# Kernel optimization log

Measured on AMD Instinct MI355X. Metric: run time of the kernel, lower is better.

## Reference

```python
import jax, jax.numpy as jnp
import numpy as np

N, T, HID, H = 2, 2048, 1024, 16
D = HID // H


def setup_inputs() -> dict:
    key = jax.random.key(0)
    ks = jax.random.split(key, 11)
    s = 1.0 / np.sqrt(HID)
    return {
        "q": jax.random.normal(ks[0], (N, T, HID), jnp.float32),
        "k": jax.random.normal(ks[1], (N, T, HID), jnp.float32),
        "v": jax.random.normal(ks[2], (N, T, HID), jnp.float32),
        "Wq": jax.random.normal(ks[3], (HID, HID), jnp.float32) * s,
        "bq": jnp.zeros((HID,), jnp.float32),
        "Wk": jax.random.normal(ks[4], (HID, HID), jnp.float32) * s,
        "bk": jnp.zeros((HID,), jnp.float32),
        "Wv": jax.random.normal(ks[5], (HID, HID), jnp.float32) * s,
        "bv": jnp.zeros((HID,), jnp.float32),
        "Wo": jax.random.normal(ks[6], (HID, HID), jnp.float32) * s,
        "bo": jnp.zeros((HID,), jnp.float32),
    }


def reference(q, k, v, Wq, bq, Wk, bk, Wv, bv, Wo, bo):
    n, t, _ = q.shape
    # Linear projections, then the original's quirky head split:
    # .view(N, H, T, D) directly from (N, T, H*D) (no transpose).
    qh = (q @ Wq + bq).reshape(n, H, t, D)
    kh = (k @ Wk + bk).reshape(n, H, t, D)
    vh = (v @ Wv + bv).reshape(n, H, t, D)
    # scores: (N, H, T, T), scaled by sqrt(hidden_size) (not head dim)
    scores = jnp.einsum("nhtd,nhsd->nhts", qh, kh) / jnp.sqrt(jnp.float32(HID))
    # faithful quirk: softmax over dim=1 (the head axis)
    attn = jax.nn.softmax(scores, axis=1)
    # dropout is identity (eval / drop_rate=0)
    out = jnp.einsum("nhts,nhsd->nhtd", attn, vh).reshape(n, t, H * D)
    return out @ Wo + bo
```

## Files before the change

kernel.cpp:

```cpp
#include <hip/hip_runtime.h>

typedef unsigned short u16;
typedef __bf16 bf16x8 __attribute__((ext_vector_type(8)));
typedef float f32x4 __attribute__((ext_vector_type(4)));

#define MFMA16 __builtin_amdgcn_mfma_f32_16x16x32_bf16

constexpr int NB = 2, TS = 2048, HD = 1024, NH = 16, DH = 64;
constexpr float SCALE = 0.03125f;

__device__ __forceinline__ u16 f2bf(float f) {
    union { float f; unsigned u; } v; v.f = f;
    unsigned r = v.u + 0x7FFFu + ((v.u >> 16) & 1u);
    return (u16)(r >> 16);
}
__device__ __forceinline__ float bf2f(u16 h) {
    union { unsigned u; float f; } v; v.u = ((unsigned)h) << 16;
    return v.f;
}
__device__ __forceinline__ bf16x8 ldb8(const u16* p) {
    return *reinterpret_cast<const bf16x8*>(p);
}
__device__ __forceinline__ void glds16(const u16* g, u16* l) {
    __builtin_amdgcn_global_load_lds(
        (const __attribute__((address_space(1))) unsigned int*)g,
        (__attribute__((address_space(3))) unsigned int*)l, 16, 0, 0);
}

__global__ __launch_bounds__(256) void to_bf16(
    const float* __restrict__ a0, const float* __restrict__ a1, const float* __restrict__ a2,
    u16* __restrict__ o0, u16* __restrict__ o1, u16* __restrict__ o2)
{
    const float* s; u16* d;
    if (blockIdx.y == 0)      { s = a0; d = o0; }
    else if (blockIdx.y == 1) { s = a1; d = o1; }
    else                      { s = a2; d = o2; }
    size_t i = ((size_t)blockIdx.x * 256 + threadIdx.x) * 8;
    float4 v0 = *reinterpret_cast<const float4*>(s + i);
    float4 v1 = *reinterpret_cast<const float4*>(s + i + 4);
    u16 t[8] = { f2bf(v0.x), f2bf(v0.y), f2bf(v0.z), f2bf(v0.w),
                 f2bf(v1.x), f2bf(v1.y), f2bf(v1.z), f2bf(v1.w) };
    *reinterpret_cast<uint4*>(d + i) = *reinterpret_cast<const uint4*>(t);
}

__global__ __launch_bounds__(256) void wtrans(
    const float* __restrict__ w0, const float* __restrict__ w1,
    const float* __restrict__ w2, const float* __restrict__ w3,
    u16* __restrict__ o0, u16* __restrict__ o1,
    u16* __restrict__ o2, u16* __restrict__ o3)
{
    const float* src; u16* dst;
    if (blockIdx.z == 0)      { src = w0; dst = o0; }
    else if (blockIdx.z == 1) { src = w1; dst = o1; }
    else if (blockIdx.z == 2) { src = w2; dst = o2; }
    else                      { src = w3; dst = o3; }
    __shared__ __align__(16) u16 tile[64 * 72];
    const int k0 = blockIdx.y * 64, n0 = blockIdx.x * 64;
    const int t = threadIdx.x, r = t >> 2, c0 = (t & 3) << 4;
#pragma unroll
    for (int j = 0; j < 4; ++j) {
        float4 v = *reinterpret_cast<const float4*>(&src[(size_t)(k0 + r) * HD + n0 + c0 + 4 * j]);
        tile[(c0 + 4 * j + 0) * 72 + r] = f2bf(v.x);
        tile[(c0 + 4 * j + 1) * 72 + r] = f2bf(v.y);
        tile[(c0 + 4 * j + 2) * 72 + r] = f2bf(v.z);
        tile[(c0 + 4 * j + 3) * 72 + r] = f2bf(v.w);
    }
    __syncthreads();
#pragma unroll
    for (int j = 0; j < 2; ++j)
        *reinterpret_cast<uint4*>(&dst[(size_t)(n0 + r) * HD + k0 + c0 + 8 * j]) =
            *reinterpret_cast<const uint4*>(&tile[r * 72 + c0 + 8 * j]);
}

template <typename OT>
__global__ __launch_bounds__(256) void gemm_bt(
    const u16* __restrict__ A, const u16* __restrict__ BT,
    const float* __restrict__ bias, OT* __restrict__ C,
    int M, int N, int K)
{
    __shared__ __align__(16) u16 As[64 * 32];
    __shared__ __align__(16) u16 Bs[128 * 32];
    const int m0 = blockIdx.y * 64, n0 = blockIdx.x * 128;
    const int tid = threadIdx.x, wid = tid >> 6, lane = tid & 63;
    const int q = lane >> 4, c = lane & 15;
    const int wm = wid >> 1, wn = wid & 1;
    const int arow = tid >> 2, acol = (tid & 3) << 3;
    f32x4 acc[2][4] = {};
    for (int k0 = 0; k0 < K; k0 += 32) {
        glds16(&A[(size_t)(m0 + arow) * K + k0 + acol], &As[tid * 8]);
        glds16(&BT[(size_t)(n0 + arow) * K + k0 + acol], &Bs[tid * 8]);
        glds16(&BT[(size_t)(n0 + 64 + arow) * K + k0 + acol], &Bs[2048 + tid * 8]);
        __syncthreads();
        bf16x8 af[2], bf[4];
#pragma unroll
        for (int jm = 0; jm < 2; ++jm) af[jm] = ldb8(&As[(wm * 32 + jm * 16 + c) * 32 + q * 8]);
#pragma unroll
        for (int jn = 0; jn < 4; ++jn) bf[jn] = ldb8(&Bs[(wn * 64 + jn * 16 + c) * 32 + q * 8]);
#pragma unroll
        for (int jm = 0; jm < 2; ++jm)
#pragma unroll
            for (int jn = 0; jn < 4; ++jn)
                acc[jm][jn] = MFMA16(af[jm], bf[jn], acc[jm][jn], 0, 0, 0);
        __syncthreads();
    }
#pragma unroll
    for (int jm = 0; jm < 2; ++jm)
#pragma unroll
        for (int jn = 0; jn < 4; ++jn) {
            int row = m0 + wm * 32 + jm * 16 + q * 4;
            int col = n0 + wn * 64 + jn * 16 + c;
            float b = bias[col];
#pragma unroll
            for (int r = 0; r < 4; ++r) {
                float v = acc[jm][jn][r] + b;
                if constexpr (sizeof(OT) == 4)
                    reinterpret_cast<float*>(C)[(size_t)(row + r) * N + col] = v;
                else
                    reinterpret_cast<u16*>(C)[(size_t)(row + r) * N + col] = f2bf(v);
            }
        }
}

__global__ __launch_bounds__(256) void vtrans(const u16* __restrict__ V, u16* __restrict__ VT)
{
    __shared__ __align__(16) u16 tile[64 * 72];
    const int nh = blockIdx.y, t0 = blockIdx.x * 64;
    const u16* src = V + (size_t)nh * TS * DH;
    u16* dst = VT + (size_t)nh * DH * TS;
    const int t = threadIdx.x, r = t >> 2, c0 = (t & 3) << 4;
    *reinterpret_cast<uint4*>(&tile[r * 72 + c0]) =
        *reinterpret_cast<const uint4*>(&src[(size_t)(t0 + r) * DH + c0]);
    *reinterpret_cast<uint4*>(&tile[r * 72 + c0 + 8]) =
        *reinterpret_cast<const uint4*>(&src[(size_t)(t0 + r) * DH + c0 + 8]);
    __syncthreads();
    const int d = t >> 2, tc = (t & 3) << 4;
    u16 tmp[16];
#pragma unroll
    for (int j = 0; j < 16; ++j) tmp[j] = tile[(tc + j) * 72 + d];
    *reinterpret_cast<uint4*>(&dst[(size_t)d * TS + t0 + tc]) = *reinterpret_cast<const uint4*>(&tmp[0]);
    *reinterpret_cast<uint4*>(&dst[(size_t)d * TS + t0 + tc + 8]) = *reinterpret_cast<const uint4*>(&tmp[8]);
}

__global__ __launch_bounds__(256) void z_kernel(
    const u16* __restrict__ Qp, const u16* __restrict__ Kp, u16* __restrict__ Zf)
{
    __shared__ __align__(16) u16 Ks[64 * 64];
    const int sb = blockIdx.x, tb = blockIdx.y, n = blockIdx.z;
    const int s0 = sb * 64, t0 = tb * 128;
    const int tid = threadIdx.x, wid = tid >> 6, lane = tid & 63;
    const int q = lane >> 4, c = lane & 15;
    const int krow = tid >> 3, kch = tid & 7;
    float zacc[2][4][4] = {};
    for (int h = 0; h < NH; ++h) {
        const u16* Qh = Qp + (size_t)(n * NH + h) * TS * DH;
        const u16* Kh = Kp + (size_t)(n * NH + h) * TS * DH;
        glds16(&Kh[(size_t)(s0 + krow) * DH + ((kch ^ (krow & 7)) << 3)], &Ks[tid * 8]);
        glds16(&Kh[(size_t)(s0 + 32 + krow) * DH + ((kch ^ (krow & 7)) << 3)], &Ks[2048 + tid * 8]);
        __syncthreads();
        bf16x8 qa[2][2], kb[4][2];
#pragma unroll
        for (int jm = 0; jm < 2; ++jm)
#pragma unroll
            for (int kf = 0; kf < 2; ++kf)
                qa[jm][kf] = ldb8(&Qh[(size_t)(t0 + wid * 32 + jm * 16 + c) * DH + kf * 32 + q * 8]);
#pragma unroll
        for (int i = 0; i < 4; ++i)
#pragma unroll
            for (int kf = 0; kf < 2; ++kf)
                kb[i][kf] = ldb8(&Ks[(i * 16 + c) * 64 + (((kf * 4 + q) ^ (c & 7)) << 3)]);
        f32x4 s_[2][4] = {};
#pragma unroll
        for (int kf = 0; kf < 2; ++kf)
#pragma unroll
            for (int jm = 0; jm < 2; ++jm)
#pragma unroll
                for (int i = 0; i < 4; ++i)
                    s_[jm][i] = MFMA16(qa[jm][kf], kb[i][kf], s_[jm][i], 0, 0, 0);
#pragma unroll
        for (int jm = 0; jm < 2; ++jm)
#pragma unroll
            for (int i = 0; i < 4; ++i)
#pragma unroll
                for (int r = 0; r < 4; ++r)
                    zacc[jm][i][r] += __expf(s_[jm][i][r] * SCALE);
        __syncthreads();
    }
    size_t chunk = ((size_t)((n * 32 + sb) * 16 + tb)) * 8192 + wid * 2048 + lane * 32;
#pragma unroll
    for (int jm = 0; jm < 2; ++jm) {
        u16 w_[16];
#pragma unroll
        for (int i = 0; i < 4; ++i)
#pragma unroll
            for (int r = 0; r < 4; ++r)
                w_[i * 4 + r] = f2bf(1.0f / zacc[jm][i][r]);
        *reinterpret_cast<uint4*>(&Zf[chunk + jm * 16])     = *reinterpret_cast<const uint4*>(&w_[0]);
        *reinterpret_cast<uint4*>(&Zf[chunk + jm * 16 + 8]) = *reinterpret_cast<const uint4*>(&w_[8]);
    }
}

__global__ __launch_bounds__(256) void attn_kernel(
    const u16* __restrict__ Qp, const u16* __restrict__ Kp, const u16* __restrict__ VT,
    const u16* __restrict__ Zf, u16* __restrict__ o2)
{
    __shared__ __align__(16) u16 Ks[64 * 64];
    __shared__ __align__(16) u16 Vs[64 * 64];
    __shared__ __align__(16) u16 Ps[128 * 72];
    const int tb = blockIdx.x, h = blockIdx.y, n = blockIdx.z;
    const int t0 = tb * 128;
    const int tid = threadIdx.x, wid = tid >> 6, lane = tid & 63;
    const int q = lane >> 4, c = lane & 15;
    const int krow = tid >> 3, kch = tid & 7;
    const size_t base = (size_t)(n * NH + h) * TS * DH;
    const u16* Qh = Qp + base; const u16* Kh = Kp + base; const u16* VTh = VT + base;
    bf16x8 qa[2][2];
#pragma unroll
    for (int jm = 0; jm < 2; ++jm)
#pragma unroll
        for (int kf = 0; kf < 2; ++kf)
            qa[jm][kf] = ldb8(&Qh[(size_t)(t0 + wid * 32 + jm * 16 + c) * DH + kf * 32 + q * 8]);
    f32x4 oacc[2][4] = {};
    for (int sb = 0; sb < 32; ++sb) {
        const int s0 = sb * 64;
        glds16(&Kh[(size_t)(s0 + krow) * DH + ((kch ^ (krow & 7)) << 3)], &Ks[tid * 8]);
        glds16(&Kh[(size_t)(s0 + 32 + krow) * DH + ((kch ^ (krow & 7)) << 3)], &Ks[2048 + tid * 8]);
        glds16(&VTh[(size_t)krow * TS + s0 + ((kch ^ (krow & 7)) << 3)], &Vs[tid * 8]);
        glds16(&VTh[(size_t)(32 + krow) * TS + s0 + ((kch ^ (krow & 7)) << 3)], &Vs[2048 + tid * 8]);
        __syncthreads();
        bf16x8 kb[4][2];
#pragma unroll
        for (int i = 0; i < 4; ++i)
#pragma unroll
            for (int kf = 0; kf < 2; ++kf)
                kb[i][kf] = ldb8(&Ks[(i * 16 + c) * 64 + (((kf * 4 + q) ^ (c & 7)) << 3)]);
        f32x4 s_[2][4] = {};
#pragma unroll
        for (int kf = 0; kf < 2; ++kf)
#pragma unroll
            for (int jm = 0; jm < 2; ++jm)
#pragma unroll
                for (int i = 0; i < 4; ++i)
                    s_[jm][i] = MFMA16(qa[jm][kf], kb[i][kf], s_[jm][i], 0, 0, 0);
        size_t chunk = ((size_t)((n * 32 + sb) * 16 + tb)) * 8192 + wid * 2048 + lane * 32;
        u16 zl[32];
        *reinterpret_cast<uint4*>(&zl[0])  = *reinterpret_cast<const uint4*>(&Zf[chunk]);
        *reinterpret_cast<uint4*>(&zl[8])  = *reinterpret_cast<const uint4*>(&Zf[chunk + 8]);
        *reinterpret_cast<uint4*>(&zl[16]) = *reinterpret_cast<const uint4*>(&Zf[chunk + 16]);
        *reinterpret_cast<uint4*>(&zl[24]) = *reinterpret_cast<const uint4*>(&Zf[chunk + 24]);
#pragma unroll
        for (int jm = 0; jm < 2; ++jm)
#pragma unroll
            for (int i = 0; i < 4; ++i)
#pragma unroll
                for (int r = 0; r < 4; ++r) {
                    float p = __expf(s_[jm][i][r] * SCALE) * bf2f(zl[jm * 16 + i * 4 + r]);
                    Ps[(wid * 32 + jm * 16 + q * 4 + r) * 72 + i * 16 + c] = f2bf(p);
                }
        bf16x8 pa[2][2], vb[4][2];
#pragma unroll
        for (int jm = 0; jm < 2; ++jm)
#pragma unroll
            for (int kf = 0; kf < 2; ++kf)
                pa[jm][kf] = ldb8(&Ps[(wid * 32 + jm * 16 + c) * 72 + kf * 32 + q * 8]);
#pragma unroll
        for (int dn = 0; dn < 4; ++dn)
#pragma unroll
            for (int kf = 0; kf < 2; ++kf)
                vb[dn][kf] = ldb8(&Vs[(dn * 16 + c) * 64 + (((kf * 4 + q) ^ (c & 7)) << 3)]);
#pragma unroll
        for (int kf = 0; kf < 2; ++kf)
#pragma unroll
            for (int jm = 0; jm < 2; ++jm)
#pragma unroll
                for (int dn = 0; dn < 4; ++dn)
                    oacc[jm][dn] = MFMA16(pa[jm][kf], vb[dn][kf], oacc[jm][dn], 0, 0, 0);
        __syncthreads();
    }
#pragma unroll
    for (int jm = 0; jm < 2; ++jm)
#pragma unroll
        for (int dn = 0; dn < 4; ++dn)
#pragma unroll
            for (int r = 0; r < 4; ++r)
                o2[base + (size_t)(t0 + wid * 32 + jm * 16 + q * 4 + r) * DH + dn * 16 + c] =
                    f2bf(oacc[jm][dn][r]);
}

extern "C" void kernel_launch(void* const* d_in, const int* in_sizes, int n_in,
                              void* d_out, int out_size, void* d_ws, size_t ws_size,
                              hipStream_t stream)
{
    const float* q  = (const float*)d_in[0];
    const float* k  = (const float*)d_in[1];
    const float* v  = (const float*)d_in[2];
    const float* Wq = (const float*)d_in[3];
    const float* bq = (const float*)d_in[4];
    const float* Wk = (const float*)d_in[5];
    const float* bk = (const float*)d_in[6];
    const float* Wv = (const float*)d_in[7];
    const float* bv = (const float*)d_in[8];
    const float* Wo = (const float*)d_in[9];
    const float* bo = (const float*)d_in[10];
    float* out = (float*)d_out;

    u16* ws  = (u16*)d_ws;
    u16* wqT = ws + 0 * 1048576;
    u16* wkT = ws + 1 * 1048576;
    u16* wvT = ws + 2 * 1048576;
    u16* woT = ws + 3 * 1048576;
    u16* S1  = ws + 4194304;
    u16* S2  = S1 + 4194304;
    u16* S3  = S2 + 4194304;
    u16* S4  = S3 + 4194304;
    u16* S5  = S4 + 4194304;
    u16* qb = S1, * kb = S2, * vb = S3;
    u16* Qp = S4, * Kp = S1, * Vp = S2;
    u16* VTb = S3, * Zf = S5, * o2 = S2;

    to_bf16<<<dim3(2048, 3), 256, 0, stream>>>(q, k, v, qb, kb, vb);
    wtrans<<<dim3(16, 16, 4), 256, 0, stream>>>(Wq, Wk, Wv, Wo, wqT, wkT, wvT, woT);
    gemm_bt<u16><<<dim3(8, 64), 256, 0, stream>>>(qb, wqT, bq, Qp, NB * TS, HD, HD);
    gemm_bt<u16><<<dim3(8, 64), 256, 0, stream>>>(kb, wkT, bk, Kp, NB * TS, HD, HD);
    gemm_bt<u16><<<dim3(8, 64), 256, 0, stream>>>(vb, wvT, bv, Vp, NB * TS, HD, HD);
    vtrans<<<dim3(32, 32), 256, 0, stream>>>(Vp, VTb);
    z_kernel<<<dim3(32, 16, 2), 256, 0, stream>>>(Qp, Kp, Zf);
    attn_kernel<<<dim3(16, 16, 2), 256, 0, stream>>>(Qp, Kp, VTb, Zf, o2);
    gemm_bt<float><<<dim3(8, 64), 256, 0, stream>>>(o2, woT, bo, out, NB * TS, HD, HD);
}
```

Measured before the change: 332.7 us.

## Batch QKV projections into one larger-tile GEMM and vectorize bf16 epilogues

Merges the three Q/K/V projection GEMMs into a single launch indexed by blockIdx.z, using 128x128 tiles with 4x4 MFMA accumulators per wave for more operand reuse. Swaps MFMA operand order so each lane holds four contiguous output columns, letting epilogues write packed bf16 pairs and float4 stores instead of scattered scalar stores. Adds a packed hardware bf16 conversion helper with a software fallback, used across the conversion, Z, P and output writes. Workspace buffers are reassigned to fit the concurrent outputs, at the cost of higher register use in the larger GEMM tile.

```diff
diff --git a/kernel.cpp b/kernel.cpp
--- a/kernel.cpp
+++ b/kernel.cpp
@@ -25,6 +25,24 @@
     __builtin_amdgcn_global_load_lds(
         (const __attribute__((address_space(1))) unsigned int*)g,
         (__attribute__((address_space(3))) unsigned int*)l, 16, 0, 0);
+}
+
+#if defined(__has_builtin)
+#  if __has_builtin(__builtin_amdgcn_cvt_pk_bf16_f32)
+#    define HAVE_PKBF16 1
+#  endif
+#endif
+#ifndef HAVE_PKBF16
+#  define HAVE_PKBF16 0
+#endif
+__device__ __forceinline__ unsigned pk2(float a, float b) {
+#if HAVE_PKBF16
+    typedef __bf16 bf16x2 __attribute__((ext_vector_type(2)));
+    bf16x2 r = __builtin_amdgcn_cvt_pk_bf16_f32(a, b);
+    return __builtin_bit_cast(unsigned, r);
+#else
+    return (unsigned)f2bf(a) | ((unsigned)f2bf(b) << 16);
+#endif
 }
 
 __global__ __launch_bounds__(256) void to_bf16(
@@ -38,9 +56,8 @@
     size_t i = ((size_t)blockIdx.x * 256 + threadIdx.x) * 8;
     float4 v0 = *reinterpret_cast<const float4*>(s + i);
     float4 v1 = *reinterpret_cast<const float4*>(s + i + 4);
-    u16 t[8] = { f2bf(v0.x), f2bf(v0.y), f2bf(v0.z), f2bf(v0.w),
-                 f2bf(v1.x), f2bf(v1.y), f2bf(v1.z), f2bf(v1.w) };
-    *reinterpret_cast<uint4*>(d + i) = *reinterpret_cast<const uint4*>(t);
+    uint4 w = { pk2(v0.x, v0.y), pk2(v0.z, v0.w), pk2(v1.x, v1.y), pk2(v1.z, v1.w) };
+    *reinterpret_cast<uint4*>(d + i) = w;
 }
 
 __global__ __launch_bounds__(256) void wtrans(
@@ -72,10 +89,60 @@
             *reinterpret_cast<const uint4*>(&tile[r * 72 + c0 + 8 * j]);
 }
 
-template <typename OT>
-__global__ __launch_bounds__(256) void gemm_bt(
+__global__ __launch_bounds__(256) void gemm_qkv(
+    const u16* __restrict__ A0, const u16* __restrict__ A1, const u16* __restrict__ A2,
+    const u16* __restrict__ B0, const u16* __restrict__ B1, const u16* __restrict__ B2,
+    const float* __restrict__ c0, const float* __restrict__ c1, const float* __restrict__ c2,
+    u16* __restrict__ C0, u16* __restrict__ C1, u16* __restrict__ C2)
+{
+    const u16 *A, *BT; const float* bias; u16* C;
+    if (blockIdx.z == 0)      { A = A0; BT = B0; bias = c0; C = C0; }
+    else if (blockIdx.z == 1) { A = A1; BT = B1; bias = c1; C = C1; }
+    else                      { A = A2; BT = B2; bias = c2; C = C2; }
+    constexpr int M = NB * TS, N = HD, K = HD;
+    __shared__ __align__(16) u16 As[128 * 32];
+    __shared__ __align__(16) u16 Bs[128 * 32];
+    const int m0 = blockIdx.y * 128, n0 = blockIdx.x * 128;
+    const int tid = threadIdx.x, wid = tid >> 6, lane = tid & 63;
+    const int q = lane >> 4, c = lane & 15;
+    const int wm = wid >> 1, wn = wid & 1;
+    const int srow = tid >> 2, scol = (tid & 3) << 3;
+    (void)M;
+    f32x4 acc[4][4] = {};
+    for (int k0 = 0; k0 < K; k0 += 32) {
+        glds16(&A[(size_t)(m0 + srow) * K + k0 + scol],       &As[tid * 8]);
+        glds16(&A[(size_t)(m0 + 64 + srow) * K + k0 + scol],  &As[2048 + tid * 8]);
+        glds16(&BT[(size_t)(n0 + srow) * K + k0 + scol],      &Bs[tid * 8]);
+        glds16(&BT[(size_t)(n0 + 64 + srow) * K + k0 + scol], &Bs[2048 + tid * 8]);
+        __syncthreads();
+        bf16x8 af[4], bf[4];
+#pragma unroll
+        for (int i = 0; i < 4; ++i)  af[i] = ldb8(&As[(wm * 64 + i * 16 + c) * 32 + q * 8]);
+#pragma unroll
+        for (int jn = 0; jn < 4; ++jn) bf[jn] = ldb8(&Bs[(wn * 64 + jn * 16 + c) * 32 + q * 8]);
+#pragma unroll
+        for (int i = 0; i < 4; ++i)
+#pragma unroll
+            for (int jn = 0; jn < 4; ++jn)
+                acc[i][jn] = MFMA16(bf[jn], af[i], acc[i][jn], 0, 0, 0);
+        __syncthreads();
+    }
+#pragma unroll
+    for (int i = 0; i < 4; ++i)
+#pragma unroll
+        for (int jn = 0; jn < 4; ++jn) {
+            int row = m0 + wm * 64 + i * 16 + c;
+            int col = n0 + wn * 64 + jn * 16 + q * 4;
+            float4 bb = *reinterpret_cast<const float4*>(&bias[col]);
+            uint2 w = { pk2(acc[i][jn][0] + bb.x, acc[i][jn][1] + bb.y),
+                        pk2(acc[i][jn][2] + bb.z, acc[i][jn][3] + bb.w) };
+            *reinterpret_cast<uint2*>(&C[(size_t)row * N + col]) = w;
+        }
+}
+
+__global__ __launch_bounds__(256) void gemm_out(
     const u16* __restrict__ A, const u16* __restrict__ BT,
-    const float* __restrict__ bias, OT* __restrict__ C,
+    const float* __restrict__ bias, float* __restrict__ C,
     int M, int N, int K)
 {
     __shared__ __align__(16) u16 As[64 * 32];
@@ -100,24 +167,19 @@
         for (int jm = 0; jm < 2; ++jm)
 #pragma unroll
             for (int jn = 0; jn < 4; ++jn)
-                acc[jm][jn] = MFMA16(af[jm], bf[jn], acc[jm][jn], 0, 0, 0);
+                acc[jm][jn] = MFMA16(bf[jn], af[jm], acc[jm][jn], 0, 0, 0);
         __syncthreads();
     }
 #pragma unroll
     for (int jm = 0; jm < 2; ++jm)
 #pragma unroll
         for (int jn = 0; jn < 4; ++jn) {
-            int row = m0 + wm * 32 + jm * 16 + q * 4;
-            int col = n0 + wn * 64 + jn * 16 + c;
-            float b = bias[col];
-#pragma unroll
-            for (int r = 0; r < 4; ++r) {
-                float v = acc[jm][jn][r] + b;
-                if constexpr (sizeof(OT) == 4)
-                    reinterpret_cast<float*>(C)[(size_t)(row + r) * N + col] = v;
-                else
-                    reinterpret_cast<u16*>(C)[(size_t)(row + r) * N + col] = f2bf(v);
-            }
+            int row = m0 + wm * 32 + jm * 16 + c;
+            int col = n0 + wn * 64 + jn * 16 + q * 4;
+            float4 bb = *reinterpret_cast<const float4*>(&bias[col]);
+            float4 v = { acc[jm][jn][0] + bb.x, acc[jm][jn][1] + bb.y,
+                         acc[jm][jn][2] + bb.z, acc[jm][jn][3] + bb.w };
+            *reinterpret_cast<float4*>(&C[(size_t)row * N + col]) = v;
         }
 }
 
@@ -175,7 +237,7 @@
             for (int jm = 0; jm < 2; ++jm)
 #pragma unroll
                 for (int i = 0; i < 4; ++i)
-                    s_[jm][i] = MFMA16(qa[jm][kf], kb[i][kf], s_[jm][i], 0, 0, 0);
+                    s_[jm][i] = MFMA16(kb[i][kf], qa[jm][kf], s_[jm][i], 0, 0, 0);
 #pragma unroll
         for (int jm = 0; jm < 2; ++jm)
 #pragma unroll
@@ -188,14 +250,14 @@
     size_t chunk = ((size_t)((n * 32 + sb) * 16 + tb)) * 8192 + wid * 2048 + lane * 32;
 #pragma unroll
     for (int jm = 0; jm < 2; ++jm) {
-        u16 w_[16];
-#pragma unroll
-        for (int i = 0; i < 4; ++i)
-#pragma unroll
-            for (int r = 0; r < 4; ++r)
-                w_[i * 4 + r] = f2bf(1.0f / zacc[jm][i][r]);
-        *reinterpret_cast<uint4*>(&Zf[chunk + jm * 16])     = *reinterpret_cast<const uint4*>(&w_[0]);
-        *reinterpret_cast<uint4*>(&Zf[chunk + jm * 16 + 8]) = *reinterpret_cast<const uint4*>(&w_[8]);
+        unsigned w32[8];
+#pragma unroll
+        for (int i = 0; i < 4; ++i) {
+            w32[i * 2 + 0] = pk2(1.0f / zacc[jm][i][0], 1.0f / zacc[jm][i][1]);
+            w32[i * 2 + 1] = pk2(1.0f / zacc[jm][i][2], 1.0f / zacc[jm][i][3]);
+        }
+        *reinterpret_cast<uint4*>(&Zf[chunk + jm * 16])     = *reinterpret_cast<const uint4*>(&w32[0]);
+        *reinterpret_cast<uint4*>(&Zf[chunk + jm * 16 + 8]) = *reinterpret_cast<const uint4*>(&w32[4]);
     }
 }
 
@@ -240,7 +302,7 @@
             for (int jm = 0; jm < 2; ++jm)
 #pragma unroll
                 for (int i = 0; i < 4; ++i)
-                    s_[jm][i] = MFMA16(qa[jm][kf], kb[i][kf], s_[jm][i], 0, 0, 0);
+                    s_[jm][i] = MFMA16(kb[i][kf], qa[jm][kf], s_[jm][i], 0, 0, 0);
         size_t chunk = ((size_t)((n * 32 + sb) * 16 + tb)) * 8192 + wid * 2048 + lane * 32;
         u16 zl[32];
         *reinterpret_cast<uint4*>(&zl[0])  = *reinterpret_cast<const uint4*>(&Zf[chunk]);
@@ -250,12 +312,14 @@
 #pragma unroll
         for (int jm = 0; jm < 2; ++jm)
 #pragma unroll
-            for (int i = 0; i < 4; ++i)
-#pragma unroll
-                for (int r = 0; r < 4; ++r) {
-                    float p = __expf(s_[jm][i][r] * SCALE) * bf2f(zl[jm * 16 + i * 4 + r]);
-                    Ps[(wid * 32 + jm * 16 + q * 4 + r) * 72 + i * 16 + c] = f2bf(p);
-                }
+            for (int i = 0; i < 4; ++i) {
+                float p0 = __expf(s_[jm][i][0] * SCALE) * bf2f(zl[jm * 16 + i * 4 + 0]);
+                float p1 = __expf(s_[jm][i][1] * SCALE) * bf2f(zl[jm * 16 + i * 4 + 1]);
+                float p2 = __expf(s_[jm][i][2] * SCALE) * bf2f(zl[jm * 16 + i * 4 + 2]);
+                float p3 = __expf(s_[jm][i][3] * SCALE) * bf2f(zl[jm * 16 + i * 4 + 3]);
+                uint2 w = { pk2(p0, p1), pk2(p2, p3) };
+                *reinterpret_cast<uint2*>(&Ps[(wid * 32 + jm * 16 + c) * 72 + i * 16 + q * 4]) = w;
+            }
         bf16x8 pa[2][2], vb[4][2];
 #pragma unroll
         for (int jm = 0; jm < 2; ++jm)
@@ -273,17 +337,19 @@
             for (int jm = 0; jm < 2; ++jm)
 #pragma unroll
                 for (int dn = 0; dn < 4; ++dn)
-                    oacc[jm][dn] = MFMA16(pa[jm][kf], vb[dn][kf], oacc[jm][dn], 0, 0, 0);
+                    oacc[jm][dn] = MFMA16(vb[dn][kf], pa[jm][kf], oacc[jm][dn], 0, 0, 0);
         __syncthreads();
     }
 #pragma unroll
     for (int jm = 0; jm < 2; ++jm)
 #pragma unroll
-        for (int dn = 0; dn < 4; ++dn)
-#pragma unroll
-            for (int r = 0; r < 4; ++r)
-                o2[base + (size_t)(t0 + wid * 32 + jm * 16 + q * 4 + r) * DH + dn * 16 + c] =
-                    f2bf(oacc[jm][dn][r]);
+        for (int dn = 0; dn < 4; ++dn) {
+            int t = t0 + wid * 32 + jm * 16 + c;
+            int d = dn * 16 + q * 4;
+            uint2 w = { pk2(oacc[jm][dn][0], oacc[jm][dn][1]),
+                        pk2(oacc[jm][dn][2], oacc[jm][dn][3]) };
+            *reinterpret_cast<uint2*>(&o2[base + (size_t)t * DH + d]) = w;
+        }
 }
 
 extern "C" void kernel_launch(void* const* d_in, const int* in_sizes, int n_in,
@@ -313,17 +379,18 @@
     u16* S3  = S2 + 4194304;
     u16* S4  = S3 + 4194304;
     u16* S5  = S4 + 4194304;
-    u16* qb = S1, * kb = S2, * vb = S3;
-    u16* Qp = S4, * Kp = S1, * Vp = S2;
-    u16* VTb = S3, * Zf = S5, * o2 = S2;
+    u16* S6  = S5 + 4194304;
+    (void)S3;
+    u16 *qb = S1, *kb = S2, *vb = S3;
+    u16 *Qp = S4, *Kp = S5, *Vp = S6;
+    u16 *VTb = S1, *Zf = S2, *o2 = S6;
 
     to_bf16<<<dim3(2048, 3), 256, 0, stream>>>(q, k, v, qb, kb, vb);
     wtrans<<<dim3(16, 16, 4), 256, 0, stream>>>(Wq, Wk, Wv, Wo, wqT, wkT, wvT, woT);
-    gemm_bt<u16><<<dim3(8, 64), 256, 0, stream>>>(qb, wqT, bq, Qp, NB * TS, HD, HD);
-    gemm_bt<u16><<<dim3(8, 64), 256, 0, stream>>>(kb, wkT, bk, Kp, NB * TS, HD, HD);
-    gemm_bt<u16><<<dim3(8, 64), 256, 0, stream>>>(vb, wvT, bv, Vp, NB * TS, HD, HD);
+    gemm_qkv<<<dim3(8, 32, 3), 256, 0, stream>>>(qb, kb, vb, wqT, wkT, wvT,
+                                                 bq, bk, bv, Qp, Kp, Vp);
     vtrans<<<dim3(32, 32), 256, 0, stream>>>(Vp, VTb);
     z_kernel<<<dim3(32, 16, 2), 256, 0, stream>>>(Qp, Kp, Zf);
     attn_kernel<<<dim3(16, 16, 2), 256, 0, stream>>>(Qp, Kp, VTb, Zf, o2);
-    gemm_bt<float><<<dim3(8, 64), 256, 0, stream>>>(o2, woT, bo, out, NB * TS, HD, HD);
-}
+    gemm_out<<<dim3(8, 64), 256, 0, stream>>>(o2, woT, bo, out, NB * TS, HD, HD);
+}
```

Result: faster. 324.0 us (-2.6%).
